# Optimization experiments

Hardware: AMD Instinct MI355X
Metric: run time of the kernel (lower is better)

Reference implementation:

```python
import jax, jax.numpy as jnp
import numpy as np

DIM = 256; HEADS = 8; HD = DIM // HEADS; WIN = 3; LOCAL = WIN * WIN
SR = 8; SHARED = 4; ROUTED = 2
B = 4; RES = 64; TBL = 4096
EPS = 1.1920929e-07  # torch.finfo(float32).eps


def _l2(x):
    return x / jnp.clip(jnp.linalg.norm(x, axis=-1, keepdims=True), EPS)


def _forward(x, relative_coords_table, q_w, q_b, kv_w, kv_b, temperature,
             query_embedding, rpb_local, learnable_tokens, learnable_bias,
             cpb1_w, cpb1_b, cpb2_w, cpb2_b, sr_w, sr_b, norm_g, norm_b,
             wg_w, wg0_w, wg1_w, proj_w, proj_b, relative_pos_index, H, W):
    B_, N, C = x.shape
    pH, pW = H // SR, W // SR
    PL = pH * pW
    _x = x.reshape(B_ * N, C)

    # ---- MoE head routing: top-k gating over routed heads ----
    gates = jax.nn.softmax(_x @ wg_w.T, axis=1)                 # (BN, n_routed)
    _, idx = jax.lax.top_k(gates, ROUTED)
    mask = jax.nn.one_hot(idx, gates.shape[1], dtype=gates.dtype).sum(axis=1)
    rg = gates * mask
    rg = rg / jnp.clip(jnp.sum(rg, axis=1, keepdims=True), EPS)
    routed_gates = rg.reshape(B_, N, -1) * ROUTED

    # ---- seq-length-scale buffer: log(local valid-window count + pool_len) ----
    r = WIN // 2
    ch = np.minimum(np.arange(H) + r, H - 1) - np.maximum(np.arange(H) - r, 0) + 1
    cw = np.minimum(np.arange(W) + r, W - 1) - np.maximum(np.arange(W) - r, 0) + 1
    sls = jnp.asarray(np.log(np.outer(ch, cw).reshape(-1, 1).astype(np.float32) + PL))

    # ---- queries ----
    q = (x @ q_w.T + q_b).reshape(B_, N, HEADS, HD).transpose(0, 2, 1, 3)
    q_norm = _l2(q)                                             # (B,h,N,d)
    q_scaled = (q_norm + query_embedding) * jax.nn.softplus(temperature) * sls

    # ---- local branch: unfold normalized k and v over 3x3 windows (zero pad) ----
    kv = x @ kv_w.T + kv_b                                      # (B,N,2C)
    k_loc = _l2(kv[..., :C].reshape(B_, N, HEADS, HD)).reshape(B_, N, C)
    kvl = jnp.concatenate([k_loc, kv[..., C:]], -1).transpose(0, 2, 1).reshape(B_, 2 * C, H, W)
    kvp = jnp.pad(kvl, ((0, 0), (0, 0), (r, r), (r, r)))
    patches = jnp.stack([kvp[:, :, i:i + H, j:j + W] for i in range(WIN) for j in range(WIN)], axis=2)
    patches = patches.reshape(B_, 2 * HEADS, HD, LOCAL, N).transpose(0, 1, 4, 2, 3)  # (B,2h,N,d,L)
    k_local, v_local = patches[:, :HEADS], patches[:, HEADS:]

    attn_local = jnp.einsum('bhnd,bhndl->bhnl', q_scaled, k_local) + rpb_local[:, None, :]

    # ---- pooled global branch ----
    x_ = x.transpose(0, 2, 1).reshape(B_, C, H, W)
    x_ = jnp.einsum('oc,bchw->bohw', sr_w, x_) + sr_b[None, :, None, None]  # 1x1 conv
    x_ = jax.nn.gelu(x_, approximate=False)
    x_ = x_.reshape(B_, C, pH, SR, pW, SR).mean((3, 5)).reshape(B_, C, PL).transpose(0, 2, 1)
    mu = x_.mean(-1, keepdims=True)
    var = ((x_ - mu) ** 2).mean(-1, keepdims=True)
    x_ = (x_ - mu) / jnp.sqrt(var + 1e-5) * norm_g + norm_b
    kvp2 = (x_ @ kv_w.T + kv_b).reshape(B_, PL, 2 * HEADS, HD).transpose(0, 2, 1, 3)
    k_pool, v_pool = kvp2[:, :HEADS], kvp2[:, HEADS:]

    cpb = jax.nn.relu(relative_coords_table @ cpb1_w.T + cpb1_b) @ cpb2_w.T + cpb2_b  # (T,h)
    pool_bias = cpb.T[:, relative_pos_index.reshape(-1)].reshape(HEADS, N, PL)
    attn_pool = jnp.einsum('bhnd,bhpd->bhnp', q_scaled, _l2(k_pool)) + pool_bias

    # ---- joint softmax over local + pooled keys ----
    attn = jax.nn.softmax(jnp.concatenate([attn_local, attn_pool], axis=-1), axis=-1)
    a_loc, a_pool = attn[..., :LOCAL], attn[..., LOCAL:]
    a_loc = jnp.einsum('bhnd,hdl->bhnl', q_norm, learnable_tokens) + learnable_bias + a_loc
    x_local = jnp.einsum('bhnl,bhndl->bhnd', a_loc, v_local)
    x_pool = jnp.einsum('bhnp,bhpd->bhnd', a_pool, v_pool)
    out = (x_local + x_pool).transpose(0, 2, 1, 3)              # (B,N,h,d)

    # ---- combine shared + routed head gates ----
    shared_gates = jax.nn.softmax(_x @ wg1_w.T, axis=1).reshape(B_, N, SHARED) * SHARED
    w0 = jax.nn.softmax(_x @ wg0_w.T, axis=1).reshape(B_, N, 2) * 2
    masked = jnp.concatenate([w0[..., 0:1] * shared_gates, w0[..., 1:2] * routed_gates], axis=-1)
    out = (masked[..., None] * out).reshape(B_, N, C)
    return out @ proj_w.T + proj_b


def setup_inputs() -> dict:
    key = jax.random.key(0)
    ks = jax.random.split(key, 20)
    H = W = RES
    N = H * W
    C = DIM
    PL = (H // SR) * (W // SR)

    def nrm(i, shape, s=0.02):
        return jax.random.normal(ks[i], shape, dtype=jnp.float32) * s

    return {
        'x': jax.random.normal(ks[0], (B, N, C), dtype=jnp.float32),
        'relative_coords_table': jax.random.normal(ks[1], (TBL, 2), dtype=jnp.float32),
        'q_w': nrm(3, (C, C)), 'q_b': jnp.zeros((C,), jnp.float32),
        'kv_w': nrm(4, (2 * C, C)), 'kv_b': jnp.zeros((2 * C,), jnp.float32),
        'temperature': jnp.full((HEADS, 1, 1), float(np.log(np.exp(1 / 0.24) - 1)), jnp.float32),
        'query_embedding': nrm(5, (HEADS, 1, HD)),
        'rpb_local': nrm(6, (HEADS, LOCAL), 0.0004),
        'learnable_tokens': nrm(7, (HEADS, HD, LOCAL)),
        'learnable_bias': jnp.zeros((HEADS, 1, LOCAL), jnp.float32),
        'cpb1_w': nrm(8, (512, 2)), 'cpb1_b': jnp.zeros((512,), jnp.float32),
        'cpb2_w': nrm(9, (HEADS, 512)), 'cpb2_b': jnp.zeros((HEADS,), jnp.float32),
        'sr_w': nrm(10, (C, C)), 'sr_b': jnp.zeros((C,), jnp.float32),
        'norm_g': jnp.ones((C,), jnp.float32), 'norm_b': jnp.zeros((C,), jnp.float32),
        'wg_w': nrm(11, (HEADS - SHARED, C)),
        'wg0_w': nrm(12, (2, C)),
        'wg1_w': nrm(13, (SHARED, C)),
        'proj_w': nrm(14, (C, C)), 'proj_b': jnp.zeros((C,), jnp.float32),
        'relative_pos_index': jax.random.randint(ks[2], (N, PL), 0, TBL, dtype=jnp.int32),
        'H': H, 'W': W,
    }


def reference(x, relative_coords_table, q_w, q_b, kv_w, kv_b, temperature,
              query_embedding, rpb_local, learnable_tokens, learnable_bias,
              cpb1_w, cpb1_b, cpb2_w, cpb2_b, sr_w, sr_b, norm_g, norm_b,
              wg_w, wg0_w, wg1_w, proj_w, proj_b, relative_pos_index, H, W):
    return _forward(x, relative_coords_table, q_w, q_b, kv_w, kv_b, temperature,
                    query_embedding, rpb_local, learnable_tokens, learnable_bias,
                    cpb1_w, cpb1_b, cpb2_w, cpb2_b, sr_w, sr_b, norm_g, norm_b,
                    wg_w, wg0_w, wg1_w, proj_w, proj_b, relative_pos_index, H, W)
```

## Files before the change

### kernel.cpp

```cpp
#include <hip/hip_runtime.h>
#include <math.h>

#define EPSF 1.1920929e-07f

typedef __attribute__((ext_vector_type(8))) short short8;
typedef __attribute__((ext_vector_type(4))) float f32x4;

static __device__ __forceinline__ unsigned short f2bf(float f) {
    unsigned int u = __float_as_uint(f);
    return (unsigned short)((u + 0x7FFFu + ((u >> 16) & 1u)) >> 16);
}
static __device__ __forceinline__ float bf2f(unsigned short u) {
    return __uint_as_float((unsigned int)u << 16);
}

__global__ __launch_bounds__(256) void prep_kernel(
    const float* __restrict__ x,
    const float* __restrict__ wg,  const float* __restrict__ wg0,
    const float* __restrict__ wg1,
    const float* __restrict__ q_w, const float* __restrict__ kv_w,
    const float* __restrict__ sr_w, const float* __restrict__ pw,
    const float* __restrict__ tbl,
    const float* __restrict__ c1w, const float* __restrict__ c1b,
    const float* __restrict__ c2w, const float* __restrict__ c2b,
    unsigned short* __restrict__ xbf, float* __restrict__ gate,
    unsigned short* __restrict__ wcat, unsigned short* __restrict__ pwbf,
    float* __restrict__ kv_wT, float* __restrict__ cpb)
{
    __shared__ float shpad[512];
    const int blk = blockIdx.x;
    const int t   = threadIdx.x;
    if (blk < 4096) {
        const int j = t & 63;
        const int row = (blk << 2) + (t >> 6);
        float4 v = *(const float4*)(x + (size_t)row*256 + j*4);
        ushort4 o;
        o.x = f2bf(v.x); o.y = f2bf(v.y); o.z = f2bf(v.z); o.w = f2bf(v.w);
        *(ushort4*)(xbf + (size_t)row*256 + j*4) = o;
        float d[10];
#pragma unroll
        for (int f = 0; f < 10; ++f) {
            const float* wf = (f < 4) ? (wg + f*256) : (f < 6) ? (wg0 + (f-4)*256)
                                                               : (wg1 + (f-6)*256);
            float4 wv = *(const float4*)(wf + j*4);
            float s = v.x*wv.x + v.y*wv.y + v.z*wv.z + v.w*wv.w;
            s += __shfl_xor(s, 32); s += __shfl_xor(s, 16); s += __shfl_xor(s, 8);
            s += __shfl_xor(s, 4);  s += __shfl_xor(s, 2);  s += __shfl_xor(s, 1);
            d[f] = s;
        }
        if (j == 0) {
            float e[4];
            float m = fmaxf(fmaxf(d[0],d[1]), fmaxf(d[2],d[3]));
            float ssum = 0.f;
            for (int i = 0; i < 4; ++i) { e[i] = expf(d[i]-m); ssum += e[i]; }
            for (int i = 0; i < 4; ++i) e[i] /= ssum;
            int i1 = 0;
            for (int i = 1; i < 4; ++i) if (e[i] > e[i1]) i1 = i;
            int i2 = -1;
            for (int i = 0; i < 4; ++i) if (i != i1 && (i2 < 0 || e[i] > e[i2])) i2 = i;
            float rs = fmaxf(e[i1] + e[i2], EPSF);
            float rg[4] = {0.f,0.f,0.f,0.f};
            rg[i1] = e[i1] / rs * 2.f;
            rg[i2] = e[i2] / rs * 2.f;
            float sh[4];
            float m1 = fmaxf(fmaxf(d[6],d[7]), fmaxf(d[8],d[9]));
            float s1 = 0.f;
            for (int i = 0; i < 4; ++i) { sh[i] = expf(d[6+i]-m1); s1 += sh[i]; }
            float mm = fmaxf(d[4], d[5]);
            float e0 = expf(d[4]-mm), e1 = expf(d[5]-mm);
            float w00 = e0/(e0+e1)*2.f, w01 = e1/(e0+e1)*2.f;
            float* gr = gate + ((size_t)row << 3);
            for (int i = 0; i < 4; ++i) gr[i]   = w00 * (sh[i]/s1*4.f);
            for (int i = 0; i < 4; ++i) gr[4+i] = w01 * rg[i];
        }
    } else if (blk < 4416) {
        const int e = ((blk - 4096)*256 + t)*4;
        if (e < 262144) {
            int n = e >> 8, k = e & 255;
            const float* src = (n < 256) ? (q_w + n*256) :
                               (n < 768) ? (kv_w + (n-256)*256) : (sr_w + (n-768)*256);
            float4 v = *(const float4*)(src + k);
            ushort4 o;
            o.x = f2bf(v.x); o.y = f2bf(v.y); o.z = f2bf(v.z); o.w = f2bf(v.w);
            *(ushort4*)(wcat + e) = o;
        } else {
            int e2 = e - 262144;
            float4 v = *(const float4*)(pw + e2);
            ushort4 o;
            o.x = f2bf(v.x); o.y = f2bf(v.y); o.z = f2bf(v.z); o.w = f2bf(v.w);
            *(ushort4*)(pwbf + e2) = o;
        }
    } else if (blk < 4544) {
        const int e = ((blk - 4416)*256 + t)*4;
        int o = e >> 8, k = e & 255;
        float4 v = *(const float4*)(kv_w + e);
        kv_wT[(k+0)*512 + o] = v.x;
        kv_wT[(k+1)*512 + o] = v.y;
        kv_wT[(k+2)*512 + o] = v.z;
        kv_wT[(k+3)*512 + o] = v.w;
    } else {
        const int r = blk - 4544;
        const float c0 = tbl[(size_t)r*2], c1 = tbl[(size_t)r*2+1];
        for (int i = t; i < 512; i += 256)
            shpad[i] = fmaxf(c0*c1w[i*2] + c1*c1w[i*2+1] + c1b[i], 0.f);
        __syncthreads();
        const int hh = t >> 5, dd = t & 31;
        float s = 0.f;
        for (int i = dd; i < 512; i += 32) s += shpad[i] * c2w[hh*512+i];
        for (int off = 16; off; off >>= 1) s += __shfl_xor(s, off, 32);
        if (dd == 0) cpb[(size_t)hh*4096 + r] = (s + c2b[hh]) * 1.44269504089f;
    }
}

__global__ __launch_bounds__(256) void gemm_mfma(
    const unsigned short* __restrict__ A,
    const unsigned short* __restrict__ W,
    const float* __restrict__ B0, const float* __restrict__ B1,
    const float* __restrict__ B2,
    int r1, int r2, int mode,
    float* __restrict__ C, int ldc,
    unsigned short* __restrict__ qkv,
    const float* __restrict__ temp, const float* __restrict__ qe)
{
    __shared__ __attribute__((aligned(16))) unsigned short Bt[64*264];
    const int m0b = blockIdx.y << 7;
    const int n0  = blockIdx.x << 6;
    const int t   = threadIdx.x;
    const int w   = t >> 6;
    const int col16 = t & 15;
    const int quad  = (t & 63) >> 4;
    const int cbase = n0 + 4*col16;

    const float* Bp; int noff;
    if (n0 < r1)      { Bp = B0; noff = 0;  }
    else if (n0 < r2) { Bp = B1; noff = r1; }
    else              { Bp = B2; noff = r2; }

    short8 afrA[8];
    {
        const unsigned short* ap = A + (size_t)(m0b + w*16 + col16)*256 + quad*8;
#pragma unroll
        for (int kk = 0; kk < 8; ++kk)
            afrA[kk] = *(const short8*)(ap + kk*32);
    }
#pragma unroll
    for (int j = 0; j < 8; ++j) {
        int ci = j*256 + t;
        int r = ci >> 5, c = ci & 31;
        uint4 bv = *(const uint4*)(W + (size_t)(n0 + r)*256 + c*8);
        *(uint4*)(Bt + r*264 + c*8) = bv;
    }
    __syncthreads();

    float4 bias4 = *(const float4*)(Bp + cbase - noff);
    float bias_c[4] = {bias4.x, bias4.y, bias4.z, bias4.w};

    const int region = n0 >> 8;
    float qe_c[4], sptv = 0.f;
    if (mode == 0 && region == 0) {
        float4 q4 = *(const float4*)(qe + cbase);
        qe_c[0]=q4.x; qe_c[1]=q4.y; qe_c[2]=q4.z; qe_c[3]=q4.w;
        sptv = log1pf(expf(temp[(cbase >> 5) & 7])) * 1.44269504089f;
    }

    auto epilogue = [&](f32x4* acc, int m0) {
        if (mode == 0) {
#pragma unroll
            for (int reg = 0; reg < 4; ++reg) {
                const int row = m0 + w*16 + quad*4 + reg;
                float v[4];
#pragma unroll
                for (int c = 0; c < 4; ++c) v[c] = acc[c][reg] + bias_c[c];
                if (region <= 1) {
                    float s = v[0]*v[0] + v[1]*v[1] + v[2]*v[2] + v[3]*v[3];
                    s += __shfl_xor(s, 1); s += __shfl_xor(s, 2);
                    s += __shfl_xor(s, 4);
                    float inv = 1.0f / fmaxf(sqrtf(s), EPSF);
#pragma unroll
                    for (int c = 0; c < 4; ++c) v[c] *= inv;
                }
                if (region == 0) {
                    int n = row & 4095;
                    int y = n >> 6, x = n & 63;
                    int cs = ((y==0||y==63)?2:3) + ((x==0||x==63)?2:3);
                    float sls = (cs == 4) ? 4.2195077052f :
                                (cs == 5) ? 4.2484952420f :
                                            4.2904594411f;
#pragma unroll
                    for (int c = 0; c < 4; ++c)
                        v[c] = (v[c] + qe_c[c]) * (sptv * sls);
                }
                if (region == 3) {
                    float4 g4;
                    g4.x = 0.5f*v[0]*(1.0f + erff(v[0]*0.70710678118654752f));
                    g4.y = 0.5f*v[1]*(1.0f + erff(v[1]*0.70710678118654752f));
                    g4.z = 0.5f*v[2]*(1.0f + erff(v[2]*0.70710678118654752f));
                    g4.w = 0.5f*v[3]*(1.0f + erff(v[3]*0.70710678118654752f));
                    *(float4*)(C + (size_t)row * ldc + cbase) = g4;
                } else {
                    ushort4 o;
                    o.x = f2bf(v[0]); o.y = f2bf(v[1]);
                    o.z = f2bf(v[2]); o.w = f2bf(v[3]);
                    *(ushort4*)(qkv + (size_t)row * 2048 + cbase) = o;
                }
            }
        } else {
#pragma unroll
            for (int reg = 0; reg < 4; ++reg) {
                const int row = m0 + w*16 + quad*4 + reg;
                float4 o4 = {acc[0][reg] + bias_c[0], acc[1][reg] + bias_c[1],
                             acc[2][reg] + bias_c[2], acc[3][reg] + bias_c[3]};
                *(float4*)(C + (size_t)row * ldc + cbase) = o4;
            }
        }
    };

    f32x4 acc[4];
#pragma unroll
    for (int ct = 0; ct < 4; ++ct) acc[ct] = (f32x4){0.f, 0.f, 0.f, 0.f};
#pragma unroll
    for (int kk = 0; kk < 8; ++kk) {
#pragma unroll
        for (int ct = 0; ct < 4; ++ct) {
            short8 bf = *(const short8*)(Bt + (4*col16 + ct)*264 + kk*32 + quad*8);
            acc[ct] = __builtin_amdgcn_mfma_f32_16x16x32_bf16(afrA[kk], bf, acc[ct], 0, 0, 0);
        }
    }
    short8 afrB[8];
    {
        const unsigned short* ap = A + (size_t)(m0b + 64 + w*16 + col16)*256 + quad*8;
#pragma unroll
        for (int kk = 0; kk < 8; ++kk)
            afrB[kk] = *(const short8*)(ap + kk*32);
    }
    epilogue(acc, m0b);

#pragma unroll
    for (int ct = 0; ct < 4; ++ct) acc[ct] = (f32x4){0.f, 0.f, 0.f, 0.f};
#pragma unroll
    for (int kk = 0; kk < 8; ++kk) {
#pragma unroll
        for (int ct = 0; ct < 4; ++ct) {
            short8 bf = *(const short8*)(Bt + (4*col16 + ct)*264 + kk*32 + quad*8);
            acc[ct] = __builtin_amdgcn_mfma_f32_16x16x32_bf16(afrB[kk], bf, acc[ct], 0, 0, 0);
        }
    }
    epilogue(acc, m0b + 64);
}

__global__ __launch_bounds__(256) void poolkv_kernel(
    const float* __restrict__ buf,
    const float* __restrict__ g, const float* __restrict__ bb,
    const float* __restrict__ kv_wT, const float* __restrict__ kv_b,
    unsigned short* __restrict__ kpb, unsigned short* __restrict__ vpb)
{
    __shared__ float xs[256];
    __shared__ float red[8];
    const int blk  = blockIdx.x;
    const int half = blk & 1;
    const int bp   = blk >> 1;
    const int b = bp >> 6, p = bp & 63;
    const int py = p >> 3, px = p & 7;
    const int t = threadIdx.x;
    const int lane = t & 63, w = t >> 6;

    float acc = 0.f;
#pragma unroll
    for (int dy = 0; dy < 8; ++dy)
#pragma unroll
        for (int dx = 0; dx < 8; ++dx) {
            int s = ((py*8+dy) << 6) + px*8 + dx;
            acc += buf[(((size_t)(b*4096+s)) << 10) + 768 + t];
        }
    acc *= (1.0f/64.0f);

    float a1 = acc, a2 = acc*acc;
    a1 += __shfl_xor(a1, 32); a2 += __shfl_xor(a2, 32);
    a1 += __shfl_xor(a1, 16); a2 += __shfl_xor(a2, 16);
    a1 += __shfl_xor(a1, 8);  a2 += __shfl_xor(a2, 8);
    a1 += __shfl_xor(a1, 4);  a2 += __shfl_xor(a2, 4);
    a1 += __shfl_xor(a1, 2);  a2 += __shfl_xor(a2, 2);
    a1 += __shfl_xor(a1, 1);  a2 += __shfl_xor(a2, 1);
    if (lane == 0) { red[w] = a1; red[4 + w] = a2; }
    __syncthreads();
    float mu = (red[0]+red[1]+red[2]+red[3]) * (1.0f/256.0f);
    float ms = (red[4]+red[5]+red[6]+red[7]) * (1.0f/256.0f);
    float rstd = rsqrtf(ms - mu*mu + 1e-5f);
    xs[t] = (acc - mu) * rstd * g[t] + bb[t];
    __syncthreads();

    float s = kv_b[half*256 + t];
    const float* wbase = kv_wT + half*256 + t;
#pragma unroll 8
    for (int k = 0; k < 256; ++k)
        s += xs[k] * wbase[(size_t)k*512];

    const int h = t >> 5, dd = t & 31;
    const size_t ob = (size_t)(b*8+h) << 11;
    if (half == 0) {
        float s2 = s*s;
        s2 += __shfl_xor(s2, 1); s2 += __shfl_xor(s2, 2);
        s2 += __shfl_xor(s2, 4); s2 += __shfl_xor(s2, 8);
        s2 += __shfl_xor(s2, 16);
        float invn = 1.0f / fmaxf(sqrtf(s2), EPSF);
        kpb[ob + ((size_t)p << 5) + dd] = f2bf(s * invn);
    } else {
        vpb[ob + ((size_t)dd << 6) + p] = f2bf(s);
    }
}

__global__ __launch_bounds__(256, 5) void attn_mfma(
    const unsigned short* __restrict__ qkv,
    unsigned short* __restrict__ ao,
    const unsigned short* __restrict__ kpb,
    const unsigned short* __restrict__ vpb,
    const float* __restrict__ cpb,
    const int*   __restrict__ rpi,
    const float* __restrict__ temp,
    const float* __restrict__ qe,
    const float* __restrict__ rpb,
    const float* __restrict__ lt,
    const float* __restrict__ lb,
    const float* __restrict__ gate)
{
    __shared__ __attribute__((aligned(16))) unsigned char SMEM[32624];
    unsigned short* U0  = (unsigned short*)SMEM;
    unsigned short* U1  = (unsigned short*)(SMEM + 8960);
    unsigned short* P   = (unsigned short*)(SMEM + 14080);
    unsigned short* LTT = (unsigned short*)(SMEM + 31488);
    float* dqvL = (float*)(SMEM + 32512);
    float* rpbL = (float*)(SMEM + 32576);

    const int tile = blockIdx.x;
    const int h    = blockIdx.y;
    const int b    = blockIdx.z;
    const int ty0  = (tile >> 3) << 3;
    const int tx0  = (tile & 7) << 3;
    const int t    = threadIdx.x;
    const int lane  = t & 63;
    const int w     = t >> 6;
    const int col16 = lane & 15;
    const int quad  = lane >> 4;
    const int s_w   = (20*w) & ~15;

    const int nq = w*16 + col16;
    const int qy = ty0 + (nq >> 3), qx = tx0 + (nq & 7);
    short8 aq = *(const short8*)(qkv +
        ((size_t)(b*4096 + ((qy<<6)|qx)))*2048 + h*32 + quad*8);

    int rpv[4][4];
#pragma unroll
    for (int ct = 0; ct < 4; ++ct) {
        int p = ct*16 + col16;
#pragma unroll
        for (int reg = 0; reg < 4; ++reg) {
            int n = w*16 + quad*4 + reg;
            int y = ty0 + (n >> 3), x = tx0 + (n & 7);
            rpv[ct][reg] = rpi[(size_t)((y << 6) | x)*64 + p];
        }
    }
    const float* cpbh = cpb + (size_t)h*4096;
    float pbias[4][4];
#pragma unroll
    for (int ct = 0; ct < 4; ++ct)
#pragma unroll
        for (int reg = 0; reg < 4; ++reg)
            pbias[ct][reg] = cpbh[rpv[ct][reg]];

    float gv[4];
#pragma unroll
    for (int reg = 0; reg < 4; ++reg) {
        int n = w*16 + quad*4 + reg;
        int y = ty0 + (n >> 3), x = tx0 + (n & 7);
        gv[reg] = gate[(((size_t)(b*4096 + ((y<<6)|x))) << 3) + h];
    }

    for (int i = t; i < 896; i += 256) {
        int r = i >> 3, sg = i & 7;
        uint2 val = {0u, 0u};
        if (r < 100) {
            int y = ty0 + r/10 - 1, x = tx0 + r%10 - 1;
            if (y >= 0 && y < 64 && x >= 0 && x < 64)
                val = *(const uint2*)(qkv +
                    (size_t)(b*4096 + ((y<<6)|x))*2048 + h*32 + 256 + sg*4);
        }
        *(uint2*)(U0 + r*40 + sg*4) = val;
    }
    {
        const unsigned short* src = kpb + (size_t)(b*8+h)*2048;
        for (int i = t; i < 512; i += 256)
            *(uint2*)(U1 + (i >> 3)*40 + (i & 7)*4) = *(const uint2*)(src + i*4);
    }
    const float spt  = log1pf(expf(temp[h]));
    const float sptL = spt * 1.44269504089f;
    if (t >= 64 && t < 80) {
        int j = t - 64;
        float s = 0.f;
        if (j < 9) {
            s = lb[h*9 + j];
            for (int dd = 0; dd < 32; ++dd)
                s -= qe[h*32+dd] * lt[(h*32+dd)*9 + j];
        }
        dqvL[j] = s;
    } else if (t >= 80 && t < 89) {
        rpbL[t-80] = rpb[h*9 + (t-80)] * 1.44269504089f;
    }
    for (int i = t; i < 512; i += 256) {
        int j = i >> 5, dd = i & 31;
        LTT[j*32 + dd] = (j < 9) ? f2bf(lt[(h*32+dd)*9 + j]) : (unsigned short)0;
    }
    __syncthreads();

    f32x4 cl[4], cp[4];
    {
        const f32x4 z = {0.f, 0.f, 0.f, 0.f};
#pragma unroll
        for (int ct = 0; ct < 4; ++ct) {
            short8 bk = *(const short8*)(U0 + (s_w + ct*16 + col16)*40 + quad*8);
            cl[ct] = __builtin_amdgcn_mfma_f32_16x16x32_bf16(aq, bk, z, 0, 0, 0);
        }
#pragma unroll
        for (int ct = 0; ct < 4; ++ct) {
            short8 bp = *(const short8*)(U1 + (ct*16 + col16)*40 + quad*8);
            cp[ct] = __builtin_amdgcn_mfma_f32_16x16x32_bf16(aq, bp, z, 0, 0, 0);
        }
    }
#pragma unroll
    for (int ct = 0; ct < 4; ++ct) {
        int hk = s_w + ct*16 + col16;
        int ky = hk / 10, kx = hk - ky*10;
#pragma unroll
        for (int reg = 0; reg < 4; ++reg) {
            int n = w*16 + quad*4 + reg;
            int dy = ky - (n >> 3), dx = kx - (n & 7);
            bool valid = (dy >= 0 && dy <= 2 && dx >= 0 && dx <= 2);
            cl[ct][reg] = valid ? (cl[ct][reg] + rpbL[dy*3 + dx]) : -1e30f;
        }
    }
#pragma unroll
    for (int ct = 0; ct < 4; ++ct)
#pragma unroll
        for (int reg = 0; reg < 4; ++reg)
            cp[ct][reg] += pbias[ct][reg];

    float inv[4];
#pragma unroll
    for (int reg = 0; reg < 4; ++reg) {
        float m = -1e30f;
#pragma unroll
        for (int ct = 0; ct < 4; ++ct) m = fmaxf(m, cl[ct][reg]);
#pragma unroll
        for (int ct = 0; ct < 4; ++ct) m = fmaxf(m, cp[ct][reg]);
        m = fmaxf(m, __shfl_xor(m, 1)); m = fmaxf(m, __shfl_xor(m, 2));
        m = fmaxf(m, __shfl_xor(m, 4)); m = fmaxf(m, __shfl_xor(m, 8));
        float s = 0.f;
#pragma unroll
        for (int ct = 0; ct < 4; ++ct) {
            float e = exp2f(cl[ct][reg] - m); cl[ct][reg] = e; s += e;
        }
#pragma unroll
        for (int ct = 0; ct < 4; ++ct) {
            float e = exp2f(cp[ct][reg] - m); cp[ct][reg] = e; s += e;
        }
        s += __shfl_xor(s, 1); s += __shfl_xor(s, 2);
        s += __shfl_xor(s, 4); s += __shfl_xor(s, 8);
        inv[reg] = 1.0f / s;
    }
#pragma unroll
    for (int ct = 0; ct < 4; ++ct)
#pragma unroll
        for (int reg = 0; reg < 4; ++reg) {
            int n = w*16 + quad*4 + reg;
            P[n*136 + ct*16 + col16] = f2bf(cl[ct][reg] * inv[reg]);
        }
#pragma unroll
    for (int ct = 0; ct < 4; ++ct)
#pragma unroll
        for (int reg = 0; reg < 4; ++reg) {
            int n = w*16 + quad*4 + reg;
            P[n*136 + 64 + ct*16 + col16] = f2bf(cp[ct][reg] * inv[reg]);
        }
    {
        const f32x4 z = {0.f, 0.f, 0.f, 0.f};
        short8 blt = *(const short8*)(LTT + col16*32 + quad*8);
        f32x4 cd = __builtin_amdgcn_mfma_f32_16x16x32_bf16(aq, blt, z, 0, 0, 0);
        if (col16 < 9) {
            const float iA = 1.0f / (sptL * 4.2195077052f);
            const float iB = 1.0f / (sptL * 4.2484952420f);
            const float iC = 1.0f / (sptL * 4.2904594411f);
            int dy = col16 / 3, dx = col16 - dy*3;
#pragma unroll
            for (int reg = 0; reg < 4; ++reg) {
                int n = w*16 + quad*4 + reg;
                int y = ty0 + (n >> 3), x = tx0 + (n & 7);
                int cs = ((y==0||y==63)?2:3) + ((x==0||x==63)?2:3);
                float isc = (cs == 4) ? iA : (cs == 5) ? iB : iC;
                float ltv = cd[reg] * isc + dqvL[col16];
                int hk = ((n >> 3) + dy)*10 + (n & 7) + dx;
                int pc = hk - s_w;
                P[n*136 + pc] = f2bf(bf2f(P[n*136 + pc]) + ltv);
            }
        }
    }
    __syncthreads();

    unsigned short* VT  = U0;
    unsigned short* VPT = U1;
    for (int i = t; i < 896; i += 256) {
        int r = i >> 3, sg = i & 7;
        uint2 val = {0u, 0u};
        if (r < 100) {
            int y = ty0 + r/10 - 1, x = tx0 + r%10 - 1;
            if (y >= 0 && y < 64 && x >= 0 && x < 64)
                val = *(const uint2*)(qkv +
                    (size_t)(b*4096 + ((y<<6)|x))*2048 + h*32 + 512 + sg*4);
        }
        int d0 = sg << 2;
        VT[(d0+0)*136 + r] = (unsigned short)(val.x & 0xffffu);
        VT[(d0+1)*136 + r] = (unsigned short)(val.x >> 16);
        VT[(d0+2)*136 + r] = (unsigned short)(val.y & 0xffffu);
        VT[(d0+3)*136 + r] = (unsigned short)(val.y >> 16);
    }
    {
        const unsigned short* vsrc = vpb + (size_t)(b*8+h)*2048;
        for (int i = t; i < 512; i += 256) {
            int d = i >> 4, p4 = (i & 15) << 2;
            *(uint2*)(VPT + d*72 + p4) = *(const uint2*)(vsrc + d*64 + p4);
        }
    }
    __syncthreads();

    f32x4 o0 = {0.f,0.f,0.f,0.f}, o1 = {0.f,0.f,0.f,0.f};
#pragma unroll
    for (int ks = 0; ks < 4; ++ks) {
        short8 a = *(const short8*)(P + (w*16 + col16)*136 + ks*32 + quad*8);
        short8 b0, b1;
        if (ks < 2) {
            b0 = *(const short8*)(VT + col16*136      + s_w + ks*32 + quad*8);
            b1 = *(const short8*)(VT + (16+col16)*136 + s_w + ks*32 + quad*8);
        } else {
            b0 = *(const short8*)(VPT + col16*72      + (ks-2)*32 + quad*8);
            b1 = *(const short8*)(VPT + (16+col16)*72 + (ks-2)*32 + quad*8);
        }
        o0 = __builtin_amdgcn_mfma_f32_16x16x32_bf16(a, b0, o0, 0, 0, 0);
        o1 = __builtin_amdgcn_mfma_f32_16x16x32_bf16(a, b1, o1, 0, 0, 0);
    }
#pragma unroll
    for (int reg = 0; reg < 4; ++reg) {
        int n = w*16 + quad*4 + reg;
        int y = ty0 + (n >> 3), x = tx0 + (n & 7);
        size_t rowo = (size_t)(b*4096 + ((y<<6)|x))*256 + h*32;
        float g = gv[reg];
        ao[rowo + col16]      = f2bf(o0[reg] * g);
        ao[rowo + 16 + col16] = f2bf(o1[reg] * g);
    }
}

extern "C" void kernel_launch(void* const* d_in, const int* in_sizes, int n_in,
                              void* d_out, int out_size, void* d_ws, size_t ws_size,
                              hipStream_t stream)
{
    const float* x    = (const float*)d_in[0];
    const float* tbl  = (const float*)d_in[1];
    const float* q_w  = (const float*)d_in[2];
    const float* q_b  = (const float*)d_in[3];
    const float* kv_w = (const float*)d_in[4];
    const float* kv_b = (const float*)d_in[5];
    const float* temp = (const float*)d_in[6];
    const float* qe   = (const float*)d_in[7];
    const float* rpb  = (const float*)d_in[8];
    const float* lt   = (const float*)d_in[9];
    const float* lb   = (const float*)d_in[10];
    const float* c1w  = (const float*)d_in[11];
    const float* c1b  = (const float*)d_in[12];
    const float* c2w  = (const float*)d_in[13];
    const float* c2b  = (const float*)d_in[14];
    const float* sr_w = (const float*)d_in[15];
    const float* sr_b = (const float*)d_in[16];
    const float* ng   = (const float*)d_in[17];
    const float* nbias= (const float*)d_in[18];
    const float* wg   = (const float*)d_in[19];
    const float* wg0  = (const float*)d_in[20];
    const float* wg1  = (const float*)d_in[21];
    const float* pw   = (const float*)d_in[22];
    const float* pb   = (const float*)d_in[23];
    const int*   rpi  = (const int*)d_in[24];
    (void)in_sizes; (void)n_in; (void)out_size; (void)ws_size;

    float* buf   = (float*)d_ws;
    unsigned short* qkvb = (unsigned short*)d_ws;
    float* xp    = buf + (size_t)16384*1024;
    float* kpoolf= xp + 65536;
    unsigned short* kpb = (unsigned short*)kpoolf;
    unsigned short* vpb = kpb + 131072;
    float* cpbb  = kpoolf + 131072;
    float* gateb = cpbb + 32768;
    float* kvwT  = gateb + 131072;
    unsigned short* xbf  = (unsigned short*)(kvwT + 131072);
    unsigned short* ao   = xbf;
    unsigned short* wcat = xbf + (size_t)16384*256;
    unsigned short* pwbf = wcat + 262144;
    float* out   = (float*)d_out;

    prep_kernel<<<8640,256,0,stream>>>(x, wg, wg0, wg1, q_w, kv_w, sr_w, pw,
                                       tbl, c1w, c1b, c2w, c2b,
                                       xbf, gateb, wcat, pwbf, kvwT, cpbb);
    gemm_mfma<<<dim3(16,128),256,0,stream>>>(xbf, wcat, q_b, kv_b, sr_b,
                                             256, 768, 0, buf, 1024,
                                             qkvb, temp, qe);
    poolkv_kernel<<<512,256,0,stream>>>(buf, ng, nbias, kvwT, kv_b, kpb, vpb);
    attn_mfma<<<dim3(64,8,4),256,0,stream>>>(qkvb, ao, kpb, vpb, cpbb, rpi,
                                             temp, qe, rpb, lt, lb, gateb);
    gemm_mfma<<<dim3(4,128),256,0,stream>>>(ao, pwbf, pb, pb, pb,
                                            1<<30, 1<<30, 1, out, 256,
                                            (unsigned short*)nullptr, nullptr, nullptr);
}
```

Before: 220.7 us.

## Restructure GEMM to keep A rows resident and loop over N tiles

The GEMM kernel switches from a 2D grid (64-column by 128-row tiles) to a 1D grid of 256 blocks. Each block now owns 64 rows of A held in registers and loops over all N tiles, prefetching the next weight tile into registers while the current one is computed. This removes repeated A fetches across column blocks and hides weight loads behind MFMA work. In exchange the grid is much smaller (256 blocks, roughly one per CU), each block runs a serial loop, and there is an extra barrier per tile.

Result: slower. 274.3 us (+24.3%).

```diff
diff --git a/kernel.cpp b/kernel.cpp
--- a/kernel.cpp
+++ b/kernel.cpp
@@ -117,53 +117,76 @@
     const unsigned short* __restrict__ W,
     const float* __restrict__ B0, const float* __restrict__ B1,
     const float* __restrict__ B2,
-    int r1, int r2, int mode,
+    int r1, int r2, int mode, int ntiles,
     float* __restrict__ C, int ldc,
     unsigned short* __restrict__ qkv,
     const float* __restrict__ temp, const float* __restrict__ qe)
 {
     __shared__ __attribute__((aligned(16))) unsigned short Bt[64*264];
-    const int m0b = blockIdx.y << 7;
-    const int n0  = blockIdx.x << 6;
-    const int t   = threadIdx.x;
-    const int w   = t >> 6;
+    const int m0 = blockIdx.x << 6;
+    const int t  = threadIdx.x;
+    const int w  = t >> 6;
     const int col16 = t & 15;
     const int quad  = (t & 63) >> 4;
-    const int cbase = n0 + 4*col16;
-
-    const float* Bp; int noff;
-    if (n0 < r1)      { Bp = B0; noff = 0;  }
-    else if (n0 < r2) { Bp = B1; noff = r1; }
-    else              { Bp = B2; noff = r2; }
-
-    short8 afrA[8];
+
+    short8 afr[8];
     {
-        const unsigned short* ap = A + (size_t)(m0b + w*16 + col16)*256 + quad*8;
+        const unsigned short* ap = A + (size_t)(m0 + w*16 + col16)*256 + quad*8;
 #pragma unroll
         for (int kk = 0; kk < 8; ++kk)
-            afrA[kk] = *(const short8*)(ap + kk*32);
-    }
-#pragma unroll
-    for (int j = 0; j < 8; ++j) {
-        int ci = j*256 + t;
-        int r = ci >> 5, c = ci & 31;
-        uint4 bv = *(const uint4*)(W + (size_t)(n0 + r)*256 + c*8);
-        *(uint4*)(Bt + r*264 + c*8) = bv;
-    }
-    __syncthreads();
-
-    float4 bias4 = *(const float4*)(Bp + cbase - noff);
-    float bias_c[4] = {bias4.x, bias4.y, bias4.z, bias4.w};
-
-    const int region = n0 >> 8;
-    float qe_c[4], sptv = 0.f;
-    if (mode == 0 && region == 0) {
-        float4 q4 = *(const float4*)(qe + cbase);
-        qe_c[0]=q4.x; qe_c[1]=q4.y; qe_c[2]=q4.z; qe_c[3]=q4.w;
-        sptv = log1pf(expf(temp[(cbase >> 5) & 7])) * 1.44269504089f;
-    }
-
-    auto epilogue = [&](f32x4* acc, int m0) {
+            afr[kk] = *(const short8*)(ap + kk*32);
+    }
+
+    const int sr_ = t >> 5;
+    const int sc_ = t & 31;
+
+    uint4 Breg[8];
+#pragma unroll
+    for (int j = 0; j < 8; ++j)
+        Breg[j] = *(const uint4*)(W + (size_t)(j*8 + sr_)*256 + sc_*8);
+
+    for (int nt = 0; nt < ntiles; ++nt) {
+        const int n0 = nt << 6;
+        const int cbase = n0 + 4*col16;
+
+#pragma unroll
+        for (int j = 0; j < 8; ++j)
+            *(uint4*)(Bt + (j*8 + sr_)*264 + sc_*8) = Breg[j];
+        __syncthreads();
+
+        if (nt + 1 < ntiles) {
+            const unsigned short* wn = W + (size_t)(nt+1)*64*256;
+#pragma unroll
+            for (int j = 0; j < 8; ++j)
+                Breg[j] = *(const uint4*)(wn + (size_t)(j*8 + sr_)*256 + sc_*8);
+        }
+
+        const float* Bp; int noff;
+        if (n0 < r1)      { Bp = B0; noff = 0;  }
+        else if (n0 < r2) { Bp = B1; noff = r1; }
+        else              { Bp = B2; noff = r2; }
+        float4 bias4 = *(const float4*)(Bp + cbase - noff);
+        float bias_c[4] = {bias4.x, bias4.y, bias4.z, bias4.w};
+        const int region = n0 >> 8;
+        float qe_c[4], sptv = 0.f;
+        if (mode == 0 && region == 0) {
+            float4 q4 = *(const float4*)(qe + cbase);
+            qe_c[0]=q4.x; qe_c[1]=q4.y; qe_c[2]=q4.z; qe_c[3]=q4.w;
+            sptv = log1pf(expf(temp[(cbase >> 5) & 7])) * 1.44269504089f;
+        }
+
+        f32x4 acc[4];
+#pragma unroll
+        for (int ct = 0; ct < 4; ++ct) acc[ct] = (f32x4){0.f, 0.f, 0.f, 0.f};
+#pragma unroll
+        for (int kk = 0; kk < 8; ++kk) {
+#pragma unroll
+            for (int ct = 0; ct < 4; ++ct) {
+                short8 bf = *(const short8*)(Bt + (4*col16 + ct)*264 + kk*32 + quad*8);
+                acc[ct] = __builtin_amdgcn_mfma_f32_16x16x32_bf16(afr[kk], bf, acc[ct], 0, 0, 0);
+            }
+        }
+
         if (mode == 0) {
 #pragma unroll
             for (int reg = 0; reg < 4; ++reg) {
@@ -213,39 +236,8 @@
                 *(float4*)(C + (size_t)row * ldc + cbase) = o4;
             }
         }
-    };
-
-    f32x4 acc[4];
-#pragma unroll
-    for (int ct = 0; ct < 4; ++ct) acc[ct] = (f32x4){0.f, 0.f, 0.f, 0.f};
-#pragma unroll
-    for (int kk = 0; kk < 8; ++kk) {
-#pragma unroll
-        for (int ct = 0; ct < 4; ++ct) {
-            short8 bf = *(const short8*)(Bt + (4*col16 + ct)*264 + kk*32 + quad*8);
-            acc[ct] = __builtin_amdgcn_mfma_f32_16x16x32_bf16(afrA[kk], bf, acc[ct], 0, 0, 0);
-        }
-    }
-    short8 afrB[8];
-    {
-        const unsigned short* ap = A + (size_t)(m0b + 64 + w*16 + col16)*256 + quad*8;
-#pragma unroll
-        for (int kk = 0; kk < 8; ++kk)
-            afrB[kk] = *(const short8*)(ap + kk*32);
-    }
-    epilogue(acc, m0b);
-
-#pragma unroll
-    for (int ct = 0; ct < 4; ++ct) acc[ct] = (f32x4){0.f, 0.f, 0.f, 0.f};
-#pragma unroll
-    for (int kk = 0; kk < 8; ++kk) {
-#pragma unroll
-        for (int ct = 0; ct < 4; ++ct) {
-            short8 bf = *(const short8*)(Bt + (4*col16 + ct)*264 + kk*32 + quad*8);
-            acc[ct] = __builtin_amdgcn_mfma_f32_16x16x32_bf16(afrB[kk], bf, acc[ct], 0, 0, 0);
-        }
-    }
-    epilogue(acc, m0b + 64);
+        __syncthreads();
+    }
 }
 
 __global__ __launch_bounds__(256) void poolkv_kernel(
@@ -605,13 +597,13 @@
     prep_kernel<<<8640,256,0,stream>>>(x, wg, wg0, wg1, q_w, kv_w, sr_w, pw,
                                        tbl, c1w, c1b, c2w, c2b,
                                        xbf, gateb, wcat, pwbf, kvwT, cpbb);
-    gemm_mfma<<<dim3(16,128),256,0,stream>>>(xbf, wcat, q_b, kv_b, sr_b,
-                                             256, 768, 0, buf, 1024,
-                                             qkvb, temp, qe);
+    gemm_mfma<<<256,256,0,stream>>>(xbf, wcat, q_b, kv_b, sr_b,
+                                    256, 768, 0, 16, buf, 1024,
+                                    qkvb, temp, qe);
     poolkv_kernel<<<512,256,0,stream>>>(buf, ng, nbias, kvwT, kv_b, kpb, vpb);
     attn_mfma<<<dim3(64,8,4),256,0,stream>>>(qkvb, ao, kpb, vpb, cpbb, rpi,
                                              temp, qe, rpb, lt, lb, gateb);
-    gemm_mfma<<<dim3(4,128),256,0,stream>>>(ao, pwbf, pb, pb, pb,
-                                            1<<30, 1<<30, 1, out, 256,
-                                            (unsigned short*)nullptr, nullptr, nullptr);
+    gemm_mfma<<<256,256,0,stream>>>(ao, pwbf, pb, pb, pb,
+                                    1<<30, 1<<30, 1, 4, out, 256,
+                                    (unsigned short*)nullptr, nullptr, nullptr);
 }
```
